# Optimization experiments

Hardware: AMD Instinct MI355X
Metric: run time of the kernel (lower is better)

## Reference

```python
import jax, jax.numpy as jnp
import numpy as np

IN_H, IN_W = 450, 450
KH, KW = 15, 15
SH, SW = 1, 1
PH, PW = 0, 0
OH = (IN_H - KH + 2 * PH) // SH + 1  # 436
OW = (IN_W - KW + 2 * PW) // SW + 1  # 436


def setup_inputs() -> dict:
    key = jax.random.key(0)
    k1, k2 = jax.random.split(key)
    x = jax.random.uniform(k1, (IN_H, IN_W), dtype=jnp.float32)
    # Untied weights: one (KH, KW) kernel per output location, matching the
    # per-column nonzeros of the original sparse weight matrix.
    W = jax.random.normal(k2, (OH, OW, KH, KW), dtype=jnp.float32)
    return {"x": x, "W": W}


def reference(x, W):
    # Equivalent to padding x, flattening, and multiplying by the huge
    # mostly-zero [(H+2p)*(W+2p), OH*OW] matrix: only the receptive-field
    # entries are nonzero, so gather patches and dot with each local kernel.
    patches = jax.lax.conv_general_dilated_patches(
        x[None, None],                 # [1, 1, IN_H, IN_W]
        filter_shape=(KH, KW),
        window_strides=(SH, SW),
        padding=[(PH, PH), (PW, PW)],
    )                                   # [1, KH*KW, OH, OW]
    out = jnp.einsum('pij,ijp->ij', patches[0], W.reshape(OH, OW, KH * KW))
    return out  # [OH, OW]
```

## Files before the change

### kernel.cpp

```cpp
#include <hip/hip_runtime.h>


constexpr int IN_H = 450, IN_W = 450;
constexpr int KH = 15, KW = 15;
constexpr int OH = 436, OW = 436;
constexpr int NOUT = OH * OW;
constexpr int KSIZE = KH * KW;
constexpr int WAVES_PER_BLOCK = 4;

__global__ __launch_bounds__(256)
void lc2d_wave_per_out(const float* __restrict__ x,
                       const float* __restrict__ W,
                       float* __restrict__ out) {
    const int lane = threadIdx.x & 63;
    const int wave = threadIdx.x >> 6;
    const int oidx = blockIdx.x * WAVES_PER_BLOCK + wave;
    if (oidx >= NOUT) return;

    const int oi = oidx / OW;
    const int oj = oidx - oi * OW;

    const float* __restrict__ wbase = W + (size_t)oidx * KSIZE;
    const float* __restrict__ xbase = x + oi * IN_W + oj;

    float sum = 0.0f;
#pragma unroll
    for (int t = 0; t < 4; ++t) {
        const int p = lane + t * 64;
        if (p < KSIZE) {
            const int kh = p / KW;
            const int kw = p - kh * KW;
            sum += wbase[p] * xbase[kh * IN_W + kw];
        }
    }

#pragma unroll
    for (int off = 32; off > 0; off >>= 1)
        sum += __shfl_down(sum, off, 64);

    if (lane == 0) out[oidx] = sum;
}

extern "C" void kernel_launch(void* const* d_in, const int* in_sizes, int n_in,
                              void* d_out, int out_size, void* d_ws, size_t ws_size,
                              hipStream_t stream) {
    const float* x = (const float*)d_in[0];
    const float* W = (const float*)d_in[1];
    float* out = (float*)d_out;

    const int nblocks = (NOUT + WAVES_PER_BLOCK - 1) / WAVES_PER_BLOCK;
    lc2d_wave_per_out<<<nblocks, 64 * WAVES_PER_BLOCK, 0, stream>>>(x, W, out);
}
```

Before: 239.7 us.

## Switch from wave-per-output to thread-per-output with serial FMA accumulation

Replaces the mapping where a 64-lane wave computes one output via a shuffle reduction with one thread per output that loops over the 15x15 window with FMAs. This removes the cross-lane reduction and the idle lanes (225 of 256 slots used). In exchange, adjacent threads read weight rows 900 bytes apart, making W loads uncoalesced and relying on caches to reuse partially fetched lines.

```diff
diff --git a/kernel.cpp b/kernel.cpp
--- a/kernel.cpp
+++ b/kernel.cpp
@@ -1,44 +1,37 @@
 #include <hip/hip_runtime.h>
 
 
-constexpr int IN_H = 450, IN_W = 450;
+constexpr int IN_W = 450;
 constexpr int KH = 15, KW = 15;
 constexpr int OH = 436, OW = 436;
 constexpr int NOUT = OH * OW;
 constexpr int KSIZE = KH * KW;
-constexpr int WAVES_PER_BLOCK = 4;
 
 __global__ __launch_bounds__(256)
-void lc2d_wave_per_out(const float* __restrict__ x,
-                       const float* __restrict__ W,
-                       float* __restrict__ out) {
-    const int lane = threadIdx.x & 63;
-    const int wave = threadIdx.x >> 6;
-    const int oidx = blockIdx.x * WAVES_PER_BLOCK + wave;
+void lc2d_thread_per_out(const float* __restrict__ x,
+                         const float* __restrict__ W,
+                         float* __restrict__ out) {
+    const int oidx = blockIdx.x * 256 + threadIdx.x;
     if (oidx >= NOUT) return;
 
     const int oi = oidx / OW;
     const int oj = oidx - oi * OW;
 
-    const float* __restrict__ wbase = W + (size_t)oidx * KSIZE;
-    const float* __restrict__ xbase = x + oi * IN_W + oj;
+    const float* __restrict__ wp = W + (size_t)oidx * KSIZE;
+    const float* __restrict__ xp = x + oi * IN_W + oj;
 
     float sum = 0.0f;
+#pragma unroll 3
+    for (int kh = 0; kh < KH; ++kh) {
+        const float* __restrict__ xr = xp + kh * IN_W;
+        const float* __restrict__ wr = wp + kh * KW;
 #pragma unroll
-    for (int t = 0; t < 4; ++t) {
-        const int p = lane + t * 64;
-        if (p < KSIZE) {
-            const int kh = p / KW;
-            const int kw = p - kh * KW;
-            sum += wbase[p] * xbase[kh * IN_W + kw];
+        for (int kw = 0; kw < KW; ++kw) {
+            sum = fmaf(wr[kw], xr[kw], sum);
         }
     }
 
-#pragma unroll
-    for (int off = 32; off > 0; off >>= 1)
-        sum += __shfl_down(sum, off, 64);
-
-    if (lane == 0) out[oidx] = sum;
+    out[oidx] = sum;
 }
 
 extern "C" void kernel_launch(void* const* d_in, const int* in_sizes, int n_in,
@@ -48,6 +41,6 @@
     const float* W = (const float*)d_in[1];
     float* out = (float*)d_out;
 
-    const int nblocks = (NOUT + WAVES_PER_BLOCK - 1) / WAVES_PER_BLOCK;
-    lc2d_wave_per_out<<<nblocks, 64 * WAVES_PER_BLOCK, 0, stream>>>(x, W, out);
+    const int nblocks = (NOUT + 255) / 256;
+    lc2d_thread_per_out<<<nblocks, 256, 0, stream>>>(x, W, out);
 }
```

Result: slower. 266.4 us (+11.2%).
